# Performance work log

Hardware: AMD Instinct MI355X
Metric: run time of the kernel (lower is better)

Reference implementation:

```python
import jax, jax.numpy as jnp
import numpy as np

B, L, DIM, HEADS, DIM_HEAD = 16, 1024, 512, 8, 64


def _make_perms(rng):
    # perm = identity on first DIM indices, random permutation of [DIM, L*DIM) after
    perms = []
    for _ in range(HEADS - 1):
        tail = rng.permutation(np.arange(DIM, L * DIM))
        perms.append(np.concatenate([np.arange(DIM), tail]))
    return jnp.asarray(np.stack(perms), dtype=jnp.int64)


def setup_inputs() -> dict:
    key = jax.random.key(0)
    ks = jax.random.split(key, 6)
    s = 0.02
    return {
        "x": jax.random.normal(ks[0], (B, L, DIM), dtype=jnp.float32),
        "perms": _make_perms(np.random.default_rng(0)),
        "Wq": jax.random.normal(ks[1], (HEADS, DIM, DIM_HEAD), dtype=jnp.float32) * s,
        "Wk": jax.random.normal(ks[2], (HEADS, DIM, DIM_HEAD), dtype=jnp.float32) * s,
        "Wv": jax.random.normal(ks[3], (HEADS, DIM, DIM_HEAD), dtype=jnp.float32) * s,
        "Wo": jax.random.normal(ks[4], (DIM, HEADS * DIM_HEAD), dtype=jnp.float32) * s,
        "bo": jnp.zeros((DIM,), dtype=jnp.float32),
    }


def reference(x, perms, Wq, Wk, Wv, Wo, bo):
    b, l, d = x.shape
    h, _, e = Wq.shape
    scale = e ** -0.5
    # shuffled query inputs for heads 1..h-1
    flat = x.reshape(b, l * d)                      # [B, L*D]
    shuf = flat[:, perms].reshape(b, h - 1, l, d)   # [B, H-1, L, D]
    xq = jnp.concatenate([x[:, None], shuf], axis=1)  # [B, H, L, D]
    q = jnp.einsum('bhld,hde->bhle', xq, Wq)
    k = jnp.einsum('bld,hde->bhle', x, Wk)
    v = jnp.einsum('bld,hde->bhle', x, Wv)
    attn = jax.nn.softmax(jnp.einsum('bhqe,bhke->bhqk', q, k) * scale, axis=-1)
    out = jnp.einsum('bhqk,bhke->bhqe', attn, v)    # [B, H, L, E]
    out = out.transpose(0, 2, 1, 3).reshape(b, l, h * e)  # concat heads on last dim
    return jnp.einsum('bli,di->bld', out, Wo) + bo
```

## Files before the change

### kernel.cpp

```cpp
#include <hip/hip_runtime.h>

#define LL 1024
#define DD 512
#define HH 8
#define EE 64
#define LDX (LL*DD)
#define BB 16

typedef _Float16 h8 __attribute__((ext_vector_type(8)));
typedef _Float16 h4 __attribute__((ext_vector_type(4)));
typedef float f4 __attribute__((ext_vector_type(4)));
typedef int i4 __attribute__((ext_vector_type(4)));

__device__ __forceinline__ f4 mfma16(h8 a, h8 b, f4 c) {
    return __builtin_amdgcn_mfma_f32_16x16x32_f16(a, b, c, 0, 0, 0);
}

__global__ __launch_bounds__(256) void k_prep_all(
    const float* __restrict__ x,  const float* __restrict__ Wq,
    const float* __restrict__ Wk, const float* __restrict__ Wv,
    const float* __restrict__ Wo,
    _Float16* __restrict__ x16, _Float16* __restrict__ xT,
    _Float16* __restrict__ WT,  _Float16* __restrict__ Wo16)
{
    const int bx = blockIdx.x;
    const int t = threadIdx.x;
    if (bx < 8192) {
        const int i = bx * 256 + t;
        f4 v = ((const f4*)x)[i];
        h4 o;
        #pragma unroll
        for (int j = 0; j < 4; ++j) o[j] = (_Float16)v[j];
        *(h4*)(x16 + 4*(size_t)i) = o;
    } else if (bx < 8192 + 2048) {
        const int s = (bx - 8192) * 256 + t;
        h8 lo, hi;
        #pragma unroll
        for (int b = 0; b < 8; ++b)  lo[b] = (_Float16)x[(size_t)b*LDX + s];
        #pragma unroll
        for (int b = 0; b < 8; ++b)  hi[b] = (_Float16)x[(size_t)(b+8)*LDX + s];
        _Float16* d = xT + (size_t)s * BB;
        *(h8*)d = lo; *(h8*)(d + 8) = hi;
    } else if (bx < 8192 + 2048 + 192) {
        const int id = bx - (8192 + 2048);
        const int d0 = (id & 7) * 64;
        const int zz = id >> 3;
        const float* src; float sc = 1.f;
        if (zz < 8)       src = Wk + (size_t)zz*DD*EE;
        else if (zz < 16) src = Wv + (size_t)(zz-8)*DD*EE;
        else            { src = Wq + (size_t)(zz-16)*DD*EE; sc = 0.18033688011112042f; }
        const int e = t & 63, dq = t >> 6;
        #pragma unroll
        for (int i = 0; i < 16; ++i) {
            int d = d0 + dq*16 + i;
            WT[(size_t)(zz*64 + e)*DD + d] = (_Float16)(src[(size_t)d*EE + e] * sc);
        }
    } else {
        const int i = (bx - (8192 + 2048 + 192)) * 256 + t;
        f4 v = ((const f4*)Wo)[i];
        #pragma unroll
        for (int j = 0; j < 4; ++j) Wo16[4*i + j] = (_Float16)v[j];
    }
}

__device__ __forceinline__ void qkv_body(
    int y, int r0,
    const _Float16* __restrict__ x16, const _Float16* __restrict__ WT,
    _Float16* __restrict__ qw, _Float16* __restrict__ kw, _Float16* __restrict__ vw,
    _Float16* smem)
{
    auto As = (_Float16(*)[128][72])smem;
    auto Bs = (_Float16(*)[128][72])(smem + 2*128*72);

    const int t = threadIdx.x;
    const int wv = t >> 6, lane = t & 63;
    const int m = lane & 15, qd = lane >> 4;
    const int sr = t >> 1, sc0 = (t & 1) * 32;

    const _Float16* ax = x16 + (size_t)(r0 + sr)*DD + sc0;
    const _Float16* bx = WT  + (size_t)(y*128 + sr)*DD + sc0;

    #pragma unroll
    for (int c = 0; c < 4; ++c) {
        *(h8*)&As[0][sr][sc0 + 8*c] = *(const h8*)(ax + 8*c);
        *(h8*)&Bs[0][sr][sc0 + 8*c] = *(const h8*)(bx + 8*c);
    }
    __syncthreads();

    f4 acc[2][8] = {};
    int cur = 0;
    for (int kt = 0; kt < 8; ++kt) {
        const int alt = cur ^ 1;
        h8 an[4], bn[4];
        if (kt < 7) {
            const _Float16* a2 = ax + (kt+1)*64;
            const _Float16* b2 = bx + (kt+1)*64;
            #pragma unroll
            for (int c = 0; c < 4; ++c) {
                an[c] = *(const h8*)(a2 + 8*c);
                bn[c] = *(const h8*)(b2 + 8*c);
            }
        }
        #pragma unroll
        for (int ks = 0; ks < 2; ++ks) {
            h8 a0 = *(const h8*)&As[cur][32*wv +  0 + m][32*ks + 8*qd];
            h8 a1 = *(const h8*)&As[cur][32*wv + 16 + m][32*ks + 8*qd];
            #pragma unroll
            for (int nt = 0; nt < 8; ++nt) {
                h8 bb = *(const h8*)&Bs[cur][16*nt + m][32*ks + 8*qd];
                acc[0][nt] = mfma16(a0, bb, acc[0][nt]);
                acc[1][nt] = mfma16(a1, bb, acc[1][nt]);
            }
        }
        if (kt < 7) {
            #pragma unroll
            for (int c = 0; c < 4; ++c) {
                *(h8*)&As[alt][sr][sc0 + 8*c] = an[c];
                *(h8*)&Bs[alt][sr][sc0 + 8*c] = bn[c];
            }
            __syncthreads();
            cur = alt;
        }
    }

    #pragma unroll
    for (int nt = 0; nt < 8; ++nt) {
        const int n = y*128 + 16*nt + m;
        const int z = n >> 6, e = n & 63;
        if (z >= 17) continue;
        _Float16* dst; int h;
        if (z < 8)       { dst = kw; h = z; }
        else if (z < 16) { dst = vw; h = z - 8; }
        else             { dst = qw; h = 0; }
        dst += (size_t)h*LL*EE + e;
        #pragma unroll
        for (int mt = 0; mt < 2; ++mt)
            #pragma unroll
            for (int r = 0; r < 4; ++r) {
                int R = r0 + 32*wv + 16*mt + 4*qd + r;
                int b = R >> 10, l = R & 1023;
                dst[((size_t)b*HH*LL + l)*EE] = (_Float16)acc[mt][nt][r];
            }
    }
}

__device__ __forceinline__ void qshuf_body(
    int l0, int h,
    const _Float16* __restrict__ xT, const int* __restrict__ perms,
    const _Float16* __restrict__ WT, _Float16* __restrict__ qw,
    _Float16* smem)
{
    auto As = (_Float16(*)[64][72])smem;
    auto Bs = (_Float16(*)[64][72])(smem + 2*64*72);

    const _Float16* Wb = WT + (size_t)((16 + h)*64)*DD;
    const int* pbase = perms + (size_t)(h-1)*LDX;

    const int t = threadIdx.x;
    const int wv = t >> 6, lane = t & 63;
    const int m = lane & 15, qd = lane >> 4;
    const int lg = t >> 6, kcol = t & 63;
    const int br = t >> 2, bc0 = (t & 3) * 16;

    int pv[8];
    #pragma unroll
    for (int kt = 0; kt < 8; ++kt)
        pv[kt] = pbase[(size_t)(l0 + lg)*DD + kt*64 + kcol];

    h8 g0p[3], g1p[3], b0p[3], b1p[3];
    #pragma unroll
    for (int j = 0; j < 3; ++j) {
        const _Float16* g = xT + (size_t)pv[j] * BB;
        g0p[j] = *(const h8*)g; g1p[j] = *(const h8*)(g + 8);
        const _Float16* s = Wb + (size_t)br*DD + j*64 + bc0;
        b0p[j] = *(const h8*)s; b1p[j] = *(const h8*)(s + 8);
    }

    *(h8*)&Bs[0][br][bc0]     = b0p[0];
    *(h8*)&Bs[0][br][bc0 + 8] = b1p[0];
    #pragma unroll
    for (int i = 0; i < 8; ++i) As[0][lg*16 + i][kcol]     = g0p[0][i];
    #pragma unroll
    for (int i = 0; i < 8; ++i) As[0][lg*16 + 8 + i][kcol] = g1p[0][i];
    __syncthreads();

    f4 acc[4] = {};
    #pragma unroll
    for (int kt = 0; kt < 8; ++kt) {
        const int cur = kt & 1;
        if (kt + 3 < 8) {
            const int st = (kt + 3) % 3;
            const _Float16* g = xT + (size_t)pv[kt+3] * BB;
            g0p[st] = *(const h8*)g; g1p[st] = *(const h8*)(g + 8);
            const _Float16* s = Wb + (size_t)br*DD + (kt+3)*64 + bc0;
            b0p[st] = *(const h8*)s; b1p[st] = *(const h8*)(s + 8);
        }
        #pragma unroll
        for (int ks = 0; ks < 2; ++ks) {
            h8 a = *(const h8*)&As[cur][16*wv + m][32*ks + 8*qd];
            #pragma unroll
            for (int nt = 0; nt < 4; ++nt) {
                h8 bb = *(const h8*)&Bs[cur][16*nt + m][32*ks + 8*qd];
                acc[nt] = mfma16(a, bb, acc[nt]);
            }
        }
        if (kt < 7) {
            const int alt = cur ^ 1;
            const int st = (kt + 1) % 3;
            *(h8*)&Bs[alt][br][bc0]     = b0p[st];
            *(h8*)&Bs[alt][br][bc0 + 8] = b1p[st];
            #pragma unroll
            for (int i = 0; i < 8; ++i) As[alt][lg*16 + i][kcol]     = g0p[st][i];
            #pragma unroll
            for (int i = 0; i < 8; ++i) As[alt][lg*16 + 8 + i][kcol] = g1p[st][i];
            __syncthreads();
        }
    }

    #pragma unroll
    for (int nt = 0; nt < 4; ++nt)
        #pragma unroll
        for (int r = 0; r < 4; ++r) {
            int b = 4*qd + r;
            qw[((size_t)(b*HH + h)*LL + l0 + wv)*EE + 16*nt + m] = (_Float16)acc[nt][r];
        }
}

__global__ __launch_bounds__(256) void k_qkv_qshuf(
    const _Float16* __restrict__ x16, const _Float16* __restrict__ xT,
    const int* __restrict__ perms, const _Float16* __restrict__ WT,
    _Float16* __restrict__ qw, _Float16* __restrict__ kw, _Float16* __restrict__ vw)
{
    __shared__ __align__(16) _Float16 smem[4*128*72];
    const int bx = blockIdx.x;
    const int lx = (bx & 7) * 368 + (bx >> 3);
    const int g = lx / 23, pos = lx % 23;
    if (pos < 9) {
        const int qid = g*9 + pos;
        qkv_body(qid % 9, (qid / 9) * 128, x16, WT, qw, kw, vw, smem);
    } else {
        const int sid = g*14 + (pos - 9);
        qshuf_body((sid & 255) * 4, (sid >> 8) + 1, xT, perms, WT, qw, smem);
    }
}

__global__ __launch_bounds__(256, 4) void k_attn(
    const _Float16* __restrict__ qw, const _Float16* __restrict__ kw,
    const _Float16* __restrict__ vw, _Float16* __restrict__ oa)
{
    const int bh = blockIdx.x;
    const int l0 = blockIdx.y * 128;
    const int b = bh >> 3, h = bh & 7;
    const _Float16* qb = qw + ((size_t)bh*LL + l0)*EE;
    const _Float16* kb = kw + (size_t)bh*LL*EE;
    const _Float16* vb = vw + (size_t)bh*LL*EE;

    __shared__ __align__(16) _Float16 KsF[2][64*64];
    __shared__ __align__(16) _Float16 VtsF[2][64*64];

    const int t = threadIdx.x;
    const int wv = t >> 6, lane = t & 63;
    const int m = lane & 15, qd = lane >> 4;
    const int m7 = m & 7;
    const int qdp = ((qd & 1) << 1) | (qd >> 1);
    const int krow = t >> 2, c0 = t & 3;
    const int vkey = t & 63, vec = t >> 6;
    const int vhi = vkey >> 3, vlo = vkey & 7;

    h8 qa[2][2];
    #pragma unroll
    for (int mt = 0; mt < 2; ++mt)
        #pragma unroll
        for (int ks = 0; ks < 2; ++ks)
            qa[mt][ks] = *(const h8*)(qb + (size_t)(32*wv + 16*mt + m)*EE + 32*ks + 8*qd);

    f4 oacc[2][4] = {};
    f4 lpacc[2] = {};
    h8 ones;
    #pragma unroll
    for (int i = 0; i < 8; ++i) ones[i] = (_Float16)1.f;

    {
        const _Float16* sk = kb + (size_t)krow*EE + 16*c0;
        h8 k0 = *(const h8*)sk, k1 = *(const h8*)(sk + 8);
        const _Float16* sv = vb + (size_t)vkey*EE + 16*vec;
        h8 v0 = *(const h8*)sv, v1 = *(const h8*)(sv + 8);
        *(h8*)&KsF[0][(krow<<6) + 8*((2*c0)     ^ (krow & 7))] = k0;
        *(h8*)&KsF[0][(krow<<6) + 8*((2*c0 + 1) ^ (krow & 7))] = k1;
        #pragma unroll
        for (int i = 0; i < 8; ++i)
            VtsF[0][((16*vec + i)<<6)     + 8*(vhi ^ i) + vlo] = v0[i];
        #pragma unroll
        for (int i = 0; i < 8; ++i)
            VtsF[0][((16*vec + 8 + i)<<6) + 8*(vhi ^ i) + vlo] = v1[i];
    }
    __syncthreads();

    for (int kt = 0; kt < 16; ++kt) {
        const int cur = kt & 1, alt = cur ^ 1;
        h8 kn0, kn1, vn0, vn1;
        if (kt < 15) {
            const _Float16* sk = kb + (size_t)((kt+1)*64 + krow)*EE + 16*c0;
            kn0 = *(const h8*)sk; kn1 = *(const h8*)(sk + 8);
            const _Float16* sv = vb + (size_t)((kt+1)*64 + vkey)*EE + 16*vec;
            vn0 = *(const h8*)sv; vn1 = *(const h8*)(sv + 8);
        }

        f4 sacc[2][4] = {};
        #pragma unroll
        for (int ks = 0; ks < 2; ++ks)
            #pragma unroll
            for (int nt = 0; nt < 4; ++nt) {
                h8 kf = *(const h8*)&KsF[cur][((16*nt + m)<<6) + 8*((4*ks + qd) ^ m7)];
                sacc[0][nt] = mfma16(kf, qa[0][ks], sacc[0][nt]);
                sacc[1][nt] = mfma16(kf, qa[1][ks], sacc[1][nt]);
            }

        unsigned E[2][4][2];
        #pragma unroll
        for (int mt = 0; mt < 2; ++mt)
            #pragma unroll
            for (int nt = 0; nt < 4; ++nt) {
                float e0 = __builtin_amdgcn_exp2f(sacc[mt][nt][0]);
                float e1 = __builtin_amdgcn_exp2f(sacc[mt][nt][1]);
                float e2 = __builtin_amdgcn_exp2f(sacc[mt][nt][2]);
                float e3 = __builtin_amdgcn_exp2f(sacc[mt][nt][3]);
                E[mt][nt][0] = __builtin_bit_cast(unsigned, __builtin_amdgcn_cvt_pkrtz(e0, e1));
                E[mt][nt][1] = __builtin_bit_cast(unsigned, __builtin_amdgcn_cvt_pkrtz(e2, e3));
            }

        h8 pa[2][2];
        #pragma unroll
        for (int mt = 0; mt < 2; ++mt)
            #pragma unroll
            for (int ks = 0; ks < 2; ++ks) {
                auto x = __builtin_amdgcn_permlane16_swap(E[mt][2*ks][0], E[mt][2*ks+1][0], false, false);
                auto y = __builtin_amdgcn_permlane16_swap(E[mt][2*ks][1], E[mt][2*ks+1][1], false, false);
                i4 pw;
                pw[0] = (int)x[0]; pw[1] = (int)y[0]; pw[2] = (int)x[1]; pw[3] = (int)y[1];
                pa[mt][ks] = __builtin_bit_cast(h8, pw);
            }

        #pragma unroll
        for (int ks = 0; ks < 2; ++ks) {
            #pragma unroll
            for (int nt = 0; nt < 4; ++nt) {
                h8 vf = *(const h8*)&VtsF[cur][((16*nt + m)<<6) + 8*((4*ks + qdp) ^ m7)];
                oacc[0][nt] = mfma16(pa[0][ks], vf, oacc[0][nt]);
                oacc[1][nt] = mfma16(pa[1][ks], vf, oacc[1][nt]);
            }
            lpacc[0] = mfma16(pa[0][ks], ones, lpacc[0]);
            lpacc[1] = mfma16(pa[1][ks], ones, lpacc[1]);
        }

        if (kt < 15) {
            *(h8*)&KsF[alt][(krow<<6) + 8*((2*c0)     ^ (krow & 7))] = kn0;
            *(h8*)&KsF[alt][(krow<<6) + 8*((2*c0 + 1) ^ (krow & 7))] = kn1;
            #pragma unroll
            for (int i = 0; i < 8; ++i)
                VtsF[alt][((16*vec + i)<<6)     + 8*(vhi ^ i) + vlo] = vn0[i];
            #pragma unroll
            for (int i = 0; i < 8; ++i)
                VtsF[alt][((16*vec + 8 + i)<<6) + 8*(vhi ^ i) + vlo] = vn1[i];
            __syncthreads();
        }
    }

    _Float16* ob = oa + ((size_t)(b*LL + l0))*(HH*EE) + h*EE;
    #pragma unroll
    for (int mt = 0; mt < 2; ++mt)
        #pragma unroll
        for (int r = 0; r < 4; ++r) {
            const float inv = __builtin_amdgcn_rcpf(lpacc[mt][r]);
            #pragma unroll
            for (int nt = 0; nt < 4; ++nt) {
                int row = 32*wv + 16*mt + 4*qd + r;
                ob[(size_t)row*(HH*EE) + 16*nt + m] = (_Float16)(oacc[mt][nt][r] * inv);
            }
        }
}

__global__ __launch_bounds__(256) void k_oproj(
    const _Float16* __restrict__ oa, const _Float16* __restrict__ Wo16,
    const float* __restrict__ bo, float* __restrict__ out)
{
    const int lid = ((int)blockIdx.x & 7) * 64 + ((int)blockIdx.x >> 3);
    const int y  = lid & 3;
    const int r0 = (lid >> 2) * 128;

    __shared__ __align__(16) _Float16 As[2][128][72];
    __shared__ __align__(16) _Float16 Bs[2][128][72];

    const int t = threadIdx.x;
    const int wv = t >> 6, lane = t & 63;
    const int m = lane & 15, qd = lane >> 4;
    const int sr = t >> 1, sc0 = (t & 1) * 32;

    const _Float16* ax = oa   + (size_t)(r0 + sr)*DD + sc0;
    const _Float16* bx = Wo16 + (size_t)(y*128 + sr)*DD + sc0;

    #pragma unroll
    for (int c = 0; c < 4; ++c) {
        *(h8*)&As[0][sr][sc0 + 8*c] = *(const h8*)(ax + 8*c);
        *(h8*)&Bs[0][sr][sc0 + 8*c] = *(const h8*)(bx + 8*c);
    }
    __syncthreads();

    f4 acc[2][8] = {};
    int cur = 0;
    for (int kt = 0; kt < 8; ++kt) {
        const int alt = cur ^ 1;
        h8 an[4], bn[4];
        if (kt < 7) {
            const _Float16* a2 = ax + (kt+1)*64;
            const _Float16* b2 = bx + (kt+1)*64;
            #pragma unroll
            for (int c = 0; c < 4; ++c) {
                an[c] = *(const h8*)(a2 + 8*c);
                bn[c] = *(const h8*)(b2 + 8*c);
            }
        }
        #pragma unroll
        for (int ks = 0; ks < 2; ++ks) {
            h8 a0 = *(const h8*)&As[cur][32*wv +  0 + m][32*ks + 8*qd];
            h8 a1 = *(const h8*)&As[cur][32*wv + 16 + m][32*ks + 8*qd];
            #pragma unroll
            for (int nt = 0; nt < 8; ++nt) {
                h8 bb = *(const h8*)&Bs[cur][16*nt + m][32*ks + 8*qd];
                acc[0][nt] = mfma16(a0, bb, acc[0][nt]);
                acc[1][nt] = mfma16(a1, bb, acc[1][nt]);
            }
        }
        if (kt < 7) {
            #pragma unroll
            for (int c = 0; c < 4; ++c) {
                *(h8*)&As[alt][sr][sc0 + 8*c] = an[c];
                *(h8*)&Bs[alt][sr][sc0 + 8*c] = bn[c];
            }
            __syncthreads();
            cur = alt;
        }
    }

    #pragma unroll
    for (int nt = 0; nt < 8; ++nt) {
        const int col = y*128 + 16*nt + m;
        const float bias = bo[col];
        #pragma unroll
        for (int mt = 0; mt < 2; ++mt)
            #pragma unroll
            for (int r = 0; r < 4; ++r) {
                int row = 32*wv + 16*mt + 4*qd + r;
                out[(size_t)(r0 + row)*DD + col] = acc[mt][nt][r] + bias;
            }
    }
}

extern "C" void kernel_launch(void* const* d_in, const int* in_sizes, int n_in,
                              void* d_out, int out_size, void* d_ws, size_t ws_size,
                              hipStream_t stream)
{
    const float* x  = (const float*)d_in[0];
    const int*   pm = (const int*)d_in[1];
    const float* Wq = (const float*)d_in[2];
    const float* Wk = (const float*)d_in[3];
    const float* Wv = (const float*)d_in[4];
    const float* Wo = (const float*)d_in[5];
    const float* bo = (const float*)d_in[6];
    float* out = (float*)d_out;

    const size_t QS = (size_t)BB * HH * LL * EE;
    _Float16* q    = (_Float16*)d_ws;
    _Float16* k    = q + QS;
    _Float16* v    = k + QS;
    _Float16* oaw  = v + QS;
    _Float16* xT   = oaw;
    _Float16* WT   = oaw + QS;
    _Float16* Wo16 = WT + (size_t)24*64*DD;
    _Float16* x16  = (_Float16*)d_out;

    k_prep_all <<<dim3(8192 + 2048 + 192 + 256), 256, 0, stream>>>(
        x, Wq, Wk, Wv, Wo, x16, xT, WT, Wo16);
    k_qkv_qshuf<<<dim3(2944),            256, 0, stream>>>(x16, xT, pm, WT, q, k, v);
    k_attn     <<<dim3(BB*HH, LL/128),   256, 0, stream>>>(q, k, v, oaw);
    k_oproj    <<<dim3(512),             256, 0, stream>>>(oaw, Wo16, bo, out);
}
```

Baseline: 254.3 us.

## Fuse fp32-to-fp16 x conversion into QKV GEMM and widen attention blocks

Removes the separate x→fp16 conversion pass in the prep kernel and instead loads fp32 x directly in the QKV GEMM, packing to fp16 when staging into shared memory. This saves a full write and re-read of x in fp16. The attention kernel now uses 512-thread blocks covering 256 query rows, so each K/V tile staged in shared memory is shared by twice as many queries and each thread loads half as much. It also raises wave priority around the MFMA sections with s_setprio. The trade-off is doubled global bytes for the A operand of the QKV GEMM, plus fewer attention blocks (512) with lower occupancy per CU.

```diff
diff --git a/kernel.cpp b/kernel.cpp
--- a/kernel.cpp
+++ b/kernel.cpp
@@ -16,24 +16,24 @@
     return __builtin_amdgcn_mfma_f32_16x16x32_f16(a, b, c, 0, 0, 0);
 }
 
+__device__ __forceinline__ h8 pack8(f4 a, f4 b) {
+    h8 o;
+    #pragma unroll
+    for (int j = 0; j < 4; ++j) { o[j] = (_Float16)a[j]; o[4+j] = (_Float16)b[j]; }
+    return o;
+}
+
 __global__ __launch_bounds__(256) void k_prep_all(
     const float* __restrict__ x,  const float* __restrict__ Wq,
     const float* __restrict__ Wk, const float* __restrict__ Wv,
     const float* __restrict__ Wo,
-    _Float16* __restrict__ x16, _Float16* __restrict__ xT,
-    _Float16* __restrict__ WT,  _Float16* __restrict__ Wo16)
+    _Float16* __restrict__ xT, _Float16* __restrict__ WT,
+    _Float16* __restrict__ Wo16)
 {
     const int bx = blockIdx.x;
     const int t = threadIdx.x;
-    if (bx < 8192) {
-        const int i = bx * 256 + t;
-        f4 v = ((const f4*)x)[i];
-        h4 o;
-        #pragma unroll
-        for (int j = 0; j < 4; ++j) o[j] = (_Float16)v[j];
-        *(h4*)(x16 + 4*(size_t)i) = o;
-    } else if (bx < 8192 + 2048) {
-        const int s = (bx - 8192) * 256 + t;
+    if (bx < 2048) {
+        const int s = bx * 256 + t;
         h8 lo, hi;
         #pragma unroll
         for (int b = 0; b < 8; ++b)  lo[b] = (_Float16)x[(size_t)b*LDX + s];
@@ -41,8 +41,8 @@
         for (int b = 0; b < 8; ++b)  hi[b] = (_Float16)x[(size_t)(b+8)*LDX + s];
         _Float16* d = xT + (size_t)s * BB;
         *(h8*)d = lo; *(h8*)(d + 8) = hi;
-    } else if (bx < 8192 + 2048 + 192) {
-        const int id = bx - (8192 + 2048);
+    } else if (bx < 2048 + 192) {
+        const int id = bx - 2048;
         const int d0 = (id & 7) * 64;
         const int zz = id >> 3;
         const float* src; float sc = 1.f;
@@ -56,7 +56,7 @@
             WT[(size_t)(zz*64 + e)*DD + d] = (_Float16)(src[(size_t)d*EE + e] * sc);
         }
     } else {
-        const int i = (bx - (8192 + 2048 + 192)) * 256 + t;
+        const int i = (bx - (2048 + 192)) * 256 + t;
         f4 v = ((const f4*)Wo)[i];
         #pragma unroll
         for (int j = 0; j < 4; ++j) Wo16[4*i + j] = (_Float16)v[j];
@@ -65,7 +65,7 @@
 
 __device__ __forceinline__ void qkv_body(
     int y, int r0,
-    const _Float16* __restrict__ x16, const _Float16* __restrict__ WT,
+    const float* __restrict__ x, const _Float16* __restrict__ WT,
     _Float16* __restrict__ qw, _Float16* __restrict__ kw, _Float16* __restrict__ vw,
     _Float16* smem)
 {
@@ -77,12 +77,14 @@
     const int m = lane & 15, qd = lane >> 4;
     const int sr = t >> 1, sc0 = (t & 1) * 32;
 
-    const _Float16* ax = x16 + (size_t)(r0 + sr)*DD + sc0;
-    const _Float16* bx = WT  + (size_t)(y*128 + sr)*DD + sc0;
+    const float*    ax = x  + (size_t)(r0 + sr)*DD + sc0;
+    const _Float16* bx = WT + (size_t)(y*128 + sr)*DD + sc0;
 
     #pragma unroll
     for (int c = 0; c < 4; ++c) {
-        *(h8*)&As[0][sr][sc0 + 8*c] = *(const h8*)(ax + 8*c);
+        f4 u = *(const f4*)(ax + 8*c);
+        f4 w = *(const f4*)(ax + 8*c + 4);
+        *(h8*)&As[0][sr][sc0 + 8*c] = pack8(u, w);
         *(h8*)&Bs[0][sr][sc0 + 8*c] = *(const h8*)(bx + 8*c);
     }
     __syncthreads();
@@ -91,14 +93,15 @@
     int cur = 0;
     for (int kt = 0; kt < 8; ++kt) {
         const int alt = cur ^ 1;
-        h8 an[4], bn[4];
+        f4 an[8]; h8 bn[4];
         if (kt < 7) {
-            const _Float16* a2 = ax + (kt+1)*64;
+            const float*    a2 = ax + (kt+1)*64;
             const _Float16* b2 = bx + (kt+1)*64;
             #pragma unroll
             for (int c = 0; c < 4; ++c) {
-                an[c] = *(const h8*)(a2 + 8*c);
-                bn[c] = *(const h8*)(b2 + 8*c);
+                an[2*c]   = *(const f4*)(a2 + 8*c);
+                an[2*c+1] = *(const f4*)(a2 + 8*c + 4);
+                bn[c]     = *(const h8*)(b2 + 8*c);
             }
         }
         #pragma unroll
@@ -115,7 +118,7 @@
         if (kt < 7) {
             #pragma unroll
             for (int c = 0; c < 4; ++c) {
-                *(h8*)&As[alt][sr][sc0 + 8*c] = an[c];
+                *(h8*)&As[alt][sr][sc0 + 8*c] = pack8(an[2*c], an[2*c+1]);
                 *(h8*)&Bs[alt][sr][sc0 + 8*c] = bn[c];
             }
             __syncthreads();
@@ -227,7 +230,7 @@
 }
 
 __global__ __launch_bounds__(256) void k_qkv_qshuf(
-    const _Float16* __restrict__ x16, const _Float16* __restrict__ xT,
+    const float* __restrict__ x, const _Float16* __restrict__ xT,
     const int* __restrict__ perms, const _Float16* __restrict__ WT,
     _Float16* __restrict__ qw, _Float16* __restrict__ kw, _Float16* __restrict__ vw)
 {
@@ -237,19 +240,19 @@
     const int g = lx / 23, pos = lx % 23;
     if (pos < 9) {
         const int qid = g*9 + pos;
-        qkv_body(qid % 9, (qid / 9) * 128, x16, WT, qw, kw, vw, smem);
+        qkv_body(qid % 9, (qid / 9) * 128, x, WT, qw, kw, vw, smem);
     } else {
         const int sid = g*14 + (pos - 9);
         qshuf_body((sid & 255) * 4, (sid >> 8) + 1, xT, perms, WT, qw, smem);
     }
 }
 
-__global__ __launch_bounds__(256, 4) void k_attn(
+__global__ __launch_bounds__(512, 2) void k_attn(
     const _Float16* __restrict__ qw, const _Float16* __restrict__ kw,
     const _Float16* __restrict__ vw, _Float16* __restrict__ oa)
 {
     const int bh = blockIdx.x;
-    const int l0 = blockIdx.y * 128;
+    const int l0 = blockIdx.y * 256;
     const int b = bh >> 3, h = bh & 7;
     const _Float16* qb = qw + ((size_t)bh*LL + l0)*EE;
     const _Float16* kb = kw + (size_t)bh*LL*EE;
@@ -263,7 +266,7 @@
     const int m = lane & 15, qd = lane >> 4;
     const int m7 = m & 7;
     const int qdp = ((qd & 1) << 1) | (qd >> 1);
-    const int krow = t >> 2, c0 = t & 3;
+    const int krow = t >> 3, c0 = t & 7;
     const int vkey = t & 63, vec = t >> 6;
     const int vhi = vkey >> 3, vlo = vkey & 7;
 
@@ -281,32 +284,29 @@
     for (int i = 0; i < 8; ++i) ones[i] = (_Float16)1.f;
 
     {
-        const _Float16* sk = kb + (size_t)krow*EE + 16*c0;
-        h8 k0 = *(const h8*)sk, k1 = *(const h8*)(sk + 8);
-        const _Float16* sv = vb + (size_t)vkey*EE + 16*vec;
-        h8 v0 = *(const h8*)sv, v1 = *(const h8*)(sv + 8);
-        *(h8*)&KsF[0][(krow<<6) + 8*((2*c0)     ^ (krow & 7))] = k0;
-        *(h8*)&KsF[0][(krow<<6) + 8*((2*c0 + 1) ^ (krow & 7))] = k1;
+        const _Float16* sk = kb + (size_t)krow*EE + 8*c0;
+        h8 k0 = *(const h8*)sk;
+        const _Float16* sv = vb + (size_t)vkey*EE + 8*vec;
+        h8 v0 = *(const h8*)sv;
+        *(h8*)&KsF[0][(krow<<6) + 8*(c0 ^ (krow & 7))] = k0;
         #pragma unroll
         for (int i = 0; i < 8; ++i)
-            VtsF[0][((16*vec + i)<<6)     + 8*(vhi ^ i) + vlo] = v0[i];
-        #pragma unroll
-        for (int i = 0; i < 8; ++i)
-            VtsF[0][((16*vec + 8 + i)<<6) + 8*(vhi ^ i) + vlo] = v1[i];
+            VtsF[0][((8*vec + i)<<6) + 8*(vhi ^ i) + vlo] = v0[i];
     }
     __syncthreads();
 
     for (int kt = 0; kt < 16; ++kt) {
         const int cur = kt & 1, alt = cur ^ 1;
-        h8 kn0, kn1, vn0, vn1;
+        h8 kn0, vn0;
         if (kt < 15) {
-            const _Float16* sk = kb + (size_t)((kt+1)*64 + krow)*EE + 16*c0;
-            kn0 = *(const h8*)sk; kn1 = *(const h8*)(sk + 8);
-            const _Float16* sv = vb + (size_t)((kt+1)*64 + vkey)*EE + 16*vec;
-            vn0 = *(const h8*)sv; vn1 = *(const h8*)(sv + 8);
+            const _Float16* sk = kb + (size_t)((kt+1)*64 + krow)*EE + 8*c0;
+            kn0 = *(const h8*)sk;
+            const _Float16* sv = vb + (size_t)((kt+1)*64 + vkey)*EE + 8*vec;
+            vn0 = *(const h8*)sv;
         }
 
         f4 sacc[2][4] = {};
+        __builtin_amdgcn_s_setprio(1);
         #pragma unroll
         for (int ks = 0; ks < 2; ++ks)
             #pragma unroll
@@ -315,6 +315,7 @@
                 sacc[0][nt] = mfma16(kf, qa[0][ks], sacc[0][nt]);
                 sacc[1][nt] = mfma16(kf, qa[1][ks], sacc[1][nt]);
             }
+        __builtin_amdgcn_s_setprio(0);
 
         unsigned E[2][4][2];
         #pragma unroll
@@ -341,6 +342,7 @@
                 pa[mt][ks] = __builtin_bit_cast(h8, pw);
             }
 
+        __builtin_amdgcn_s_setprio(1);
         #pragma unroll
         for (int ks = 0; ks < 2; ++ks) {
             #pragma unroll
@@ -352,16 +354,13 @@
             lpacc[0] = mfma16(pa[0][ks], ones, lpacc[0]);
             lpacc[1] = mfma16(pa[1][ks], ones, lpacc[1]);
         }
+        __builtin_amdgcn_s_setprio(0);
 
         if (kt < 15) {
-            *(h8*)&KsF[alt][(krow<<6) + 8*((2*c0)     ^ (krow & 7))] = kn0;
-            *(h8*)&KsF[alt][(krow<<6) + 8*((2*c0 + 1) ^ (krow & 7))] = kn1;
+            *(h8*)&KsF[alt][(krow<<6) + 8*(c0 ^ (krow & 7))] = kn0;
             #pragma unroll
             for (int i = 0; i < 8; ++i)
-                VtsF[alt][((16*vec + i)<<6)     + 8*(vhi ^ i) + vlo] = vn0[i];
-            #pragma unroll
-            for (int i = 0; i < 8; ++i)
-                VtsF[alt][((16*vec + 8 + i)<<6) + 8*(vhi ^ i) + vlo] = vn1[i];
+                VtsF[alt][((8*vec + i)<<6) + 8*(vhi ^ i) + vlo] = vn0[i];
             __syncthreads();
         }
     }
@@ -477,11 +476,10 @@
     _Float16* xT   = oaw;
     _Float16* WT   = oaw + QS;
     _Float16* Wo16 = WT + (size_t)24*64*DD;
-    _Float16* x16  = (_Float16*)d_out;
-
-    k_prep_all <<<dim3(8192 + 2048 + 192 + 256), 256, 0, stream>>>(
-        x, Wq, Wk, Wv, Wo, x16, xT, WT, Wo16);
-    k_qkv_qshuf<<<dim3(2944),            256, 0, stream>>>(x16, xT, pm, WT, q, k, v);
-    k_attn     <<<dim3(BB*HH, LL/128),   256, 0, stream>>>(q, k, v, oaw);
-    k_oproj    <<<dim3(512),             256, 0, stream>>>(oaw, Wo16, bo, out);
-}
+
+    k_prep_all <<<dim3(2048 + 192 + 256), 256, 0, stream>>>(
+        x, Wq, Wk, Wv, Wo, xT, WT, Wo16);
+    k_qkv_qshuf<<<dim3(2944),          256, 0, stream>>>(x, xT, pm, WT, q, k, v);
+    k_attn     <<<dim3(BB*HH, LL/256), 512, 0, stream>>>(q, k, v, oaw);
+    k_oproj    <<<dim3(512),           256, 0, stream>>>(oaw, Wo16, bo, out);
+}
```

New measurement: 266.2 us. +4.7%, slower.
